# Optimization experiments

Hardware: AMD Instinct MI355X
Metric: run time of the kernel (lower is better)

## Reference

```python
import jax, jax.numpy as jnp
import numpy as np

NUM_CLASSES = 80
SCORE_THR = 0.2
NMS_THR = 0.3
MAX_PER_IMAGE = 100
TOPK_PER_CLASS = 100  # cap on pre-NMS candidates per (image, class); >= max_per_image
ANCHOR_MASK = [[6, 7, 8], [3, 4, 5], [0, 1, 2]]
COCO_ANCHORS = np.array([[10, 13], [16, 30], [33, 23], [30, 61], [62, 45],
                         [59, 119], [116, 90], [156, 198], [373, 326]], dtype=np.float32)


def yolo_head(feats, layer_anchors, num_classes, input_shape):
    # feats: [B, 3*(5+C), gh, gw]
    B = feats.shape[0]
    gh, gw = feats.shape[2], feats.shape[3]
    na = layer_anchors.shape[0]
    f = feats.reshape(B, na, num_classes + 5, gh, gw).transpose(0, 3, 4, 1, 2)  # [B,gh,gw,3,5+C]
    gy, gx = jnp.meshgrid(jnp.arange(gh), jnp.arange(gw), indexing='ij')
    grid = jnp.stack([gx, gy], axis=-1).astype(f.dtype)[None, :, :, None, :]  # [1,gh,gw,1,2]
    # literal translation: divide by tensor([gh, gw]) (square grids in practice)
    box_xy = (jax.nn.sigmoid(f[..., :2]) + grid) / jnp.array([gh, gw], f.dtype)
    box_wh = jnp.exp(f[..., 2:4]) * layer_anchors[None, None, None, :, :] / input_shape[None, None, None, None, :]
    conf = jax.nn.sigmoid(f[..., 4:5])
    probs = jax.nn.sigmoid(f[..., 5:])
    return box_xy, box_wh, conf, probs


def yolo_correct_boxes(box_xy, box_wh, input_shape, image_shape):
    box_yx = box_xy[..., ::-1]
    box_hw = box_wh[..., ::-1]
    new_shape = jnp.round(image_shape * jnp.min(input_shape / image_shape))
    offset = (input_shape - new_shape) / 2.0 / input_shape
    scale = input_shape / new_shape
    box_yx = (box_yx - offset) * scale
    box_hw = box_hw * scale
    mins = box_yx - box_hw / 2.0
    maxes = box_yx + box_hw / 2.0
    boxes = jnp.concatenate([mins, maxes], axis=-1)  # (ymin, xmin, ymax, xmax)
    return boxes * jnp.concatenate([image_shape, image_shape])


def decode_layer(feats, layer_anchors, input_shape, image_shape):
    box_xy, box_wh, conf, probs = yolo_head(feats, layer_anchors, NUM_CLASSES, input_shape)
    boxes = yolo_correct_boxes(box_xy, box_wh, input_shape, image_shape)  # [B,gh,gw,3,4]
    B = feats.shape[0]
    return boxes.reshape(B, -1, 4), (conf * probs).reshape(B, -1, NUM_CLASSES)


def pairwise_iou(b):
    # b: [K,4] (y1,x1,y2,x2)
    y1, x1, y2, x2 = b[:, 0], b[:, 1], b[:, 2], b[:, 3]
    area = jnp.maximum(y2 - y1, 0) * jnp.maximum(x2 - x1, 0)
    iy1 = jnp.maximum(y1[:, None], y1[None, :])
    ix1 = jnp.maximum(x1[:, None], x1[None, :])
    iy2 = jnp.minimum(y2[:, None], y2[None, :])
    ix2 = jnp.minimum(x2[:, None], x2[None, :])
    inter = jnp.maximum(iy2 - iy1, 0) * jnp.maximum(ix2 - ix1, 0)
    return inter / (area[:, None] + area[None, :] - inter + 1e-9)


def greedy_nms(boxes, valid):
    # boxes [K,4] sorted by descending score; valid [K] bool. Returns keep mask [K].
    K = boxes.shape[0]
    iou = jax.lax.stop_gradient(pairwise_iou(boxes))
    idx = jnp.arange(K)
    def body(i, sup):
        keep_i = valid[i] & (~sup[i])
        return sup | (keep_i & (iou[i] > NMS_THR) & (idx > i))
    sup = jax.lax.fori_loop(0, K, body, jnp.zeros((K,), bool))
    return valid & (~sup)


def setup_inputs() -> dict:
    key = jax.random.key(0)
    k0, k1, k2 = jax.random.split(key, 3)
    B, F = 16, 3 * (5 + NUM_CLASSES)
    feat0 = jax.random.normal(k0, (B, F, 19, 19), jnp.float32)
    feat1 = jax.random.normal(k1, (B, F, 38, 38), jnp.float32)
    feat2 = jax.random.normal(k2, (B, F, 76, 76), jnp.float32)
    anchors = jnp.asarray(COCO_ANCHORS)
    image_shape = jnp.array([480.0, 640.0], jnp.float32)
    return {"feat0": feat0, "feat1": feat1, "feat2": feat2,
            "anchors": anchors, "image_shape": image_shape}


def reference(feat0, feat1, feat2, anchors, image_shape):
    input_shape = jnp.array([feat0.shape[2] * 32, feat0.shape[3] * 32], jnp.float32)
    feats = [feat0, feat1, feat2]
    boxes_l, scores_l = [], []
    for l in range(3):
        b, s = decode_layer(feats[l], anchors[np.array(ANCHOR_MASK[l])], input_shape, image_shape)
        boxes_l.append(b)
        scores_l.append(s)
    boxes = jnp.concatenate(boxes_l, axis=1)    # [B,N,4]
    scores = jnp.concatenate(scores_l, axis=1)  # [B,N,C]
    B = scores.shape[0]
    sc = scores.transpose(0, 2, 1)              # [B,C,N]
    top_s, top_i = jax.lax.top_k(sc, TOPK_PER_CLASS)              # [B,C,K]
    top_b = jnp.take_along_axis(boxes[:, None, :, :], top_i[..., None], axis=2)  # [B,C,K,4]
    valid = top_s >= SCORE_THR
    keep = jax.vmap(jax.vmap(greedy_nms))(top_b, valid)           # [B,C,K]
    cand = jnp.where(keep, top_s, -1.0)
    flat_s = cand.reshape(B, -1)                 # [B, C*K]
    flat_b = top_b.reshape(B, -1, 4)
    sel_s, sel_i = jax.lax.top_k(flat_s, MAX_PER_IMAGE)           # [B,100]
    sel_b = jnp.take_along_axis(flat_b, sel_i[..., None], axis=1)  # [B,100,4]
    sel_c = (sel_i // TOPK_PER_CLASS).astype(jnp.float32)
    # dets: (ymin, xmin, ymax, xmax, score, class); score == -1 marks padding
    return jnp.concatenate([sel_b, sel_s[..., None], sel_c[..., None]], axis=-1)
```

## Files before the change

kernel.cpp:

```cpp
#include <hip/hip_runtime.h>
#include <hip/hip_bf16.h>


#define NTOT   22743
#define NCLS   80
#define TOPK   100
#define KPAD   22752
#define NG2    2166
#define Q_L1   17328
#define Q_L0   21660
#define SCORE_THR 0.2f
#define NMS_THR   0.3f

__device__ __forceinline__ float sig_exact(float x) {
    return 1.0f / (1.0f + expf(-x));
}
__device__ __forceinline__ float sig_fast(float x) {
    return __builtin_amdgcn_rcpf(1.0f + __expf(-x));
}

__global__ __launch_bounds__(256) void k_decode(
    const float* __restrict__ f0, const float* __restrict__ f1,
    const float* __restrict__ f2, const float* __restrict__ anchors,
    const float* __restrict__ imshape, float4* __restrict__ boxes,
    float* __restrict__ conf_q, int total) {
    int gid = blockIdx.x * 256 + threadIdx.x;
    if (gid >= total) return;
    int b = gid / NTOT; int p = gid - b * NTOT;

    const float* f; int ghw, gw, l, off, a, s;
    if (p < 1083)      { f=f0; off=0;    ghw=361;  gw=19; l=0; int r=p;      a=r/361;  s=r-a*361;  }
    else if (p < 5415) { f=f1; off=1083; ghw=1444; gw=38; l=1; int r=p-1083; a=r/1444; s=r-a*1444; }
    else               { f=f2; off=5415; ghw=5776; gw=76; l=2; int r=p-5415; a=r/5776; s=r-a*5776; }
    int y = s / gw, x = s - y * gw;

    const float* q = f + ((size_t)(b * 255 + a * 85) * ghw + s);
    float tx = q[0], ty = q[ghw], tw = q[2*ghw], th = q[3*ghw], tc = q[4*ghw];

    int arow = (2 - l) * 3 + a;
    float aw = anchors[arow * 2], ah = anchors[arow * 2 + 1];
    float imh = imshape[0], imw = imshape[1];
    float gf = (float)gw;

    float bxx = (sig_exact(tx) + (float)x) / gf;
    float bxy = (sig_exact(ty) + (float)y) / gf;
    float bw  = expf(tw) * aw / 608.0f;
    float bh  = expf(th) * ah / 608.0f;

    float r  = fminf(608.0f / imh, 608.0f / imw);
    float nh = rintf(imh * r), nw = rintf(imw * r);
    float offy = (608.0f - nh) / 2.0f / 608.0f;
    float offx = (608.0f - nw) / 2.0f / 608.0f;
    float scy = 608.0f / nh, scx = 608.0f / nw;

    float cy = (bxy - offy) * scy;
    float cx = (bxx - offx) * scx;
    float hh = bh * scy, ww = bw * scx;

    int n = off + 3 * s + a;
    boxes[(size_t)b * NTOT + n] =
        make_float4((cy - hh / 2.0f) * imh, (cx - ww / 2.0f) * imw,
                    (cy + hh / 2.0f) * imh, (cx + ww / 2.0f) * imw);
    int qi = (l == 2) ? (a * 5776 + s)
           : (l == 1) ? (Q_L1 + a * 1444 + s)
                      : (Q_L0 + a * 361 + s);
    conf_q[(size_t)b * KPAD + qi] = sig_exact(tc);
}

__device__ void find_pivot(unsigned* hist, int H, unsigned target,
                           unsigned* suf, unsigned* sh_p, unsigned* sh_above) {
    const int tid = threadIdx.x;
    const int per = H >> 8;
    if (tid < 256) {
        unsigned acc = 0;
        for (int u = 0; u < per; ++u) acc += hist[tid * per + u];
        suf[tid] = acc;
    }
    __syncthreads();
    for (int off = 1; off < 256; off <<= 1) {
        unsigned v = 0;
        if (tid < 256) v = (tid + off < 256) ? suf[tid + off] : 0u;
        __syncthreads();
        if (tid < 256) suf[tid] += v;
        __syncthreads();
    }
    if (tid < 256) {
        unsigned mysuf = suf[tid];
        unsigned nxt = (tid == 255) ? 0u : suf[tid + 1];
        if (mysuf >= target && nxt < target) {
            unsigned above = nxt;
            for (int h = tid * per + per - 1; h >= tid * per; --h) {
                unsigned c2 = above + hist[h];
                if (c2 >= target) { *sh_p = (unsigned)h; *sh_above = above; break; }
                above = c2;
            }
        }
    }
    __syncthreads();
}

__device__ __forceinline__ unsigned pack2(float cfa, float lga, float cfb, float lgb) {
    unsigned ka = __float_as_uint(cfa * sig_fast(lga)) >> 16;
    unsigned kb = __float_as_uint(cfb * sig_fast(lgb)) >> 16;
    return ka | (kb << 16);
}

__device__ __forceinline__ void collect_cand(
    int b, int c, int q, const float* __restrict__ f0,
    const float* __restrict__ f1, const float* __restrict__ f2,
    const float* __restrict__ conf_q, unsigned long long* buf,
    unsigned* sh_cnt) {
    int a, s, nbase, ghw;
    const float* f;
    if (q < Q_L1)      { a = q / 5776;  s = q - a * 5776;  f = f2; ghw = 5776; nbase = 5415; }
    else if (q < Q_L0) { int r = q - Q_L1; a = r / 1444; s = r - a * 1444; f = f1; ghw = 1444; nbase = 1083; }
    else               { int r = q - Q_L0; a = r / 361;  s = r - a * 361;  f = f0; ghw = 361;  nbase = 0;    }
    float t  = f[((size_t)(b * 255 + a * 85 + 5 + c)) * ghw + s];
    float cf = conf_q[(size_t)b * KPAD + q];
    float sce = cf * sig_exact(t);
    int n = nbase + 3 * s + a;
    unsigned slot = atomicAdd(sh_cnt, 1u);
    if (slot < 512)
        buf[slot] = (((unsigned long long)__float_as_uint(sce)) << 32)
                    | (unsigned)(~n);
}

__global__ __launch_bounds__(512, 4) void k_topk(
    const float* __restrict__ f0, const float* __restrict__ f1,
    const float* __restrict__ f2, const float* __restrict__ conf_q,
    const float4* __restrict__ boxes, float4* __restrict__ top_b,
    float* __restrict__ cand) {
    __shared__ unsigned int histp[4096];
    __shared__ unsigned long long buf[512];
    __shared__ unsigned int wsum[4];
    __shared__ float sb_y1[TOPK], sb_x1[TOPK], sb_y2[TOPK], sb_x2[TOPK], sb_s[TOPK];
    __shared__ unsigned int sh_p, sh_cnt;

    const int tid = threadIdx.x;
    const int row = blockIdx.x;
    const int b = row / NCLS, c = row - b * NCLS;
    const float* cq = conf_q + (size_t)b * KPAD;

    for (int i = tid; i < 4096; i += 512) histp[i] = 0;
    if (tid == 0) sh_cnt = 0;

    uint4 v[5];
    bool  val[5];
    float4 lg0[5], lg1[5], cf0[5], cf1[5];
    #pragma unroll
    for (int k = 0; k < 5; ++k) {
        int g = tid + k * 512;
        val[k] = (g < NG2);
        if (val[k]) {
            int q = g * 8;
            int a = q / 5776, s = q - a * 5776;
            const float* fp = f2 + ((size_t)(b * 255 + a * 85 + 5 + c)) * 5776 + s;
            lg0[k] = *(const float4*)fp;
            lg1[k] = *(const float4*)(fp + 4);
            cf0[k] = *(const float4*)(cq + q);
            cf1[k] = *(const float4*)(cq + q + 4);
        }
    }
    #pragma unroll
    for (int k = 0; k < 5; ++k) {
        if (val[k]) {
            v[k].x = pack2(cf0[k].x, lg0[k].x, cf0[k].y, lg0[k].y);
            v[k].y = pack2(cf0[k].z, lg0[k].z, cf0[k].w, lg0[k].w);
            v[k].z = pack2(cf1[k].x, lg1[k].x, cf1[k].y, lg1[k].y);
            v[k].w = pack2(cf1[k].z, lg1[k].z, cf1[k].w, lg1[k].w);
        } else v[k] = make_uint4(0, 0, 0, 0);
    }

    const bool lv = (tid < 361);
    unsigned k1p[6];
    if (lv) {
        float4 l1g[3], l1c[3];
        #pragma unroll
        for (int p = 0; p < 3; ++p) {
            const float* fp = f1 + ((size_t)(b * 255 + p * 85 + 5 + c)) * 1444 + 4 * tid;
            l1g[p] = *(const float4*)fp;
            l1c[p] = *(const float4*)(cq + Q_L1 + p * 1444 + 4 * tid);
        }
        #pragma unroll
        for (int p = 0; p < 3; ++p) {
            k1p[2*p]   = pack2(l1c[p].x, l1g[p].x, l1c[p].y, l1g[p].y);
            k1p[2*p+1] = pack2(l1c[p].z, l1g[p].z, l1c[p].w, l1g[p].w);
        }
    }

    unsigned k0[3];
    if (lv) {
        float g0f[3], c0f[3];
        #pragma unroll
        for (int p = 0; p < 3; ++p) {
            g0f[p] = f0[((size_t)(b * 255 + p * 85 + 5 + c)) * 361 + tid];
            c0f[p] = cq[Q_L0 + p * 361 + tid];
        }
        #pragma unroll
        for (int p = 0; p < 3; ++p)
            k0[p] = __float_as_uint(c0f[p] * sig_fast(g0f[p])) >> 16;
    }
    __syncthreads();

    #pragma unroll
    for (int k = 0; k < 5; ++k) if (val[k]) {
        unsigned ks[8] = { v[k].x & 0xFFFFu, v[k].x >> 16, v[k].y & 0xFFFFu, v[k].y >> 16,
                           v[k].z & 0xFFFFu, v[k].z >> 16, v[k].w & 0xFFFFu, v[k].w >> 16 };
        #pragma unroll
        for (int j = 0; j < 8; ++j)
            atomicAdd(&histp[ks[j] >> 2], 1u << (((ks[j] >> 1) & 1u) * 16));
    }
    if (lv) {
        #pragma unroll
        for (int p = 0; p < 3; ++p) {
            unsigned ks[4] = { k1p[2*p] & 0xFFFFu, k1p[2*p] >> 16,
                               k1p[2*p+1] & 0xFFFFu, k1p[2*p+1] >> 16 };
            #pragma unroll
            for (int j = 0; j < 4; ++j)
                atomicAdd(&histp[ks[j] >> 2], 1u << (((ks[j] >> 1) & 1u) * 16));
            atomicAdd(&histp[k0[p] >> 2], 1u << (((k0[p] >> 1) & 1u) * 16));
        }
    }
    __syncthreads();

    {
        const int lane = tid & 63;
        unsigned own = 0;
        if (tid < 256) {
            #pragma unroll
            for (int u = 0; u < 16; ++u) {
                unsigned w = histp[tid * 16 + u];
                own += (w & 0xFFFFu) + (w >> 16);
            }
        }
        unsigned acc = own;
        #pragma unroll
        for (int d = 1; d < 64; d <<= 1) {
            unsigned vv = __shfl_down(acc, d, 64);
            if (lane + d < 64) acc += vv;
        }
        if (tid < 256 && lane == 0) wsum[tid >> 6] = acc;
        __syncthreads();
        if (tid < 256) {
            unsigned tail = 0;
            for (int w2 = (tid >> 6) + 1; w2 < 4; ++w2) tail += wsum[w2];
            unsigned suft = acc + tail;
            unsigned nxt  = suft - own;
            if (suft >= TOPK && nxt < TOPK) {
                unsigned above = nxt;
                for (int bb = 31; bb >= 0; --bb) {
                    unsigned w = histp[tid * 16 + (bb >> 1)];
                    unsigned cnt = (bb & 1) ? (w >> 16) : (w & 0xFFFFu);
                    if (above + cnt >= TOPK) { sh_p = (unsigned)(tid * 32 + bb); break; }
                    above += cnt;
                }
            }
        }
        __syncthreads();
    }
    const unsigned kthr = sh_p > 0 ? ((sh_p - 1) << 1) : 0u;

    #pragma unroll
    for (int k = 0; k < 5; ++k) if (val[k]) {
        unsigned ks[8] = { v[k].x & 0xFFFFu, v[k].x >> 16, v[k].y & 0xFFFFu, v[k].y >> 16,
                           v[k].z & 0xFFFFu, v[k].z >> 16, v[k].w & 0xFFFFu, v[k].w >> 16 };
        #pragma unroll
        for (int j = 0; j < 8; ++j)
            if (ks[j] >= kthr)
                collect_cand(b, c, (tid + k * 512) * 8 + j, f0, f1, f2, conf_q, buf, &sh_cnt);
    }
    if (lv) {
        #pragma unroll
        for (int p = 0; p < 3; ++p) {
            unsigned ks[4] = { k1p[2*p] & 0xFFFFu, k1p[2*p] >> 16,
                               k1p[2*p+1] & 0xFFFFu, k1p[2*p+1] >> 16 };
            #pragma unroll
            for (int j = 0; j < 4; ++j)
                if (ks[j] >= kthr)
                    collect_cand(b, c, Q_L1 + p * 1444 + 4 * tid + j, f0, f1, f2, conf_q, buf, &sh_cnt);
            if (k0[p] >= kthr)
                collect_cand(b, c, Q_L0 + p * 361 + tid, f0, f1, f2, conf_q, buf, &sh_cnt);
        }
    }
    __syncthreads();

    const int M = (int)min(sh_cnt, 512u);
    if (tid < M) {
        unsigned long long mykey = buf[tid];
        int rank = 0;
        for (int j = 0; j < M; ++j) rank += (buf[j] > mykey);
        if (rank < TOPK) {
            int n = (int)(~(unsigned)mykey);
            float4 bx = boxes[(size_t)b * NTOT + n];
            sb_y1[rank] = bx.x; sb_x1[rank] = bx.y;
            sb_y2[rank] = bx.z; sb_x2[rank] = bx.w;
            sb_s[rank]  = __uint_as_float((unsigned)(mykey >> 32));
            top_b[(size_t)row * TOPK + rank] = bx;
        }
    }
    __syncthreads();

    if (tid < 64) {
        const int j0 = tid, j1 = tid + 64;
        const bool v1 = (j1 < TOPK);
        float y10 = sb_y1[j0], x10 = sb_x1[j0], y20 = sb_y2[j0], x20 = sb_x2[j0];
        float s0 = sb_s[j0];
        float y11 = v1 ? sb_y1[j1] : 0.f, x11 = v1 ? sb_x1[j1] : 0.f;
        float y21 = v1 ? sb_y2[j1] : 0.f, x21 = v1 ? sb_x2[j1] : 0.f;
        float s1 = v1 ? sb_s[j1] : -1.0f;
        float ar0 = fmaxf(y20 - y10, 0.f) * fmaxf(x20 - x10, 0.f);
        float ar1 = fmaxf(y21 - y11, 0.f) * fmaxf(x21 - x11, 0.f);
        int sup0 = 0, sup1 = 0;
        for (int i = 0; i < TOPK; ++i) {
            float yi1 = sb_y1[i], xi1 = sb_x1[i], yi2 = sb_y2[i], xi2 = sb_x2[i];
            float si = sb_s[i];
            int supi = (i < 64) ? __shfl(sup0, i, 64) : __shfl(sup1, i - 64, 64);
            bool keep_i = (si >= SCORE_THR) && (supi == 0);
            if (keep_i) {
                float ari = fmaxf(yi2 - yi1, 0.f) * fmaxf(xi2 - xi1, 0.f);
                if (j0 > i) {
                    float ty1 = fmaxf(yi1, y10), tx1 = fmaxf(xi1, x10);
                    float ty2 = fminf(yi2, y20), tx2 = fminf(xi2, x20);
                    float inter = fmaxf(ty2 - ty1, 0.f) * fmaxf(tx2 - tx1, 0.f);
                    float iou = inter / (ari + ar0 - inter + 1e-9f);
                    if (iou > NMS_THR) sup0 = 1;
                }
                if (v1 && j1 > i) {
                    float ty1 = fmaxf(yi1, y11), tx1 = fmaxf(xi1, x11);
                    float ty2 = fminf(yi2, y21), tx2 = fminf(xi2, x21);
                    float inter = fmaxf(ty2 - ty1, 0.f) * fmaxf(tx2 - tx1, 0.f);
                    float iou = inter / (ari + ar1 - inter + 1e-9f);
                    if (iou > NMS_THR) sup1 = 1;
                }
            }
        }
        cand[(size_t)row * TOPK + j0] = (s0 >= SCORE_THR && sup0 == 0) ? s0 : -1.0f;
        if (v1)
            cand[(size_t)row * TOPK + j1] = (s1 >= SCORE_THR && sup1 == 0) ? s1 : -1.0f;
    }
}

__global__ __launch_bounds__(256) void k_final(
    const float* __restrict__ cand, const float4* __restrict__ top_b,
    float* __restrict__ out) {
    __shared__ float cs[8000];
    __shared__ unsigned int hist[4096];
    __shared__ unsigned long long buf[512];
    __shared__ unsigned int suf[256];
    __shared__ unsigned int sh_kp, sh_p1, sh_above1, sh_p2, sh_above2, sh_cnt;

    const int tid = threadIdx.x, b = blockIdx.x;
    if (tid == 0) { sh_kp = 0; sh_cnt = 0; }
    for (int i = tid; i < 4096; i += 256) hist[i] = 0;
    __syncthreads();

    unsigned lk = 0;
    for (int i = tid; i < 8000; i += 256) {
        float v = cand[b * 8000 + i];
        cs[i] = v;
        if (v > -0.5f) lk++;
    }
    atomicAdd(&sh_kp, lk);
    __syncthreads();
    unsigned Kp = sh_kp;

    if (Kp >= TOPK) {
        for (int i = tid; i < 8000; i += 256)
            if (cs[i] > -0.5f) atomicAdd(&hist[__float_as_uint(cs[i]) >> 19], 1u);
        __syncthreads();
        find_pivot(hist, 2048, TOPK, suf, &sh_p1, &sh_above1);
        unsigned p1 = sh_p1, above1 = sh_above1;
        for (int i = tid; i < 4096; i += 256) hist[i] = 0;
        __syncthreads();
        for (int i = tid; i < 8000; i += 256) {
            float v = cs[i];
            if (v > -0.5f) {
                unsigned bits = __float_as_uint(v);
                if ((bits >> 19) == p1) atomicAdd(&hist[(bits >> 7) & 0xFFFu], 1u);
            }
        }
        __syncthreads();
        find_pivot(hist, 4096, TOPK - above1, suf, &sh_p2, &sh_above2);
        unsigned p2 = sh_p2;
        for (int i = tid; i < 8000; i += 256) {
            float v = cs[i];
            if (v > -0.5f) {
                unsigned bits = __float_as_uint(v);
                unsigned b1 = bits >> 19;
                if (b1 > p1 || (b1 == p1 && ((bits >> 7) & 0xFFFu) >= p2)) {
                    unsigned slot = atomicAdd(&sh_cnt, 1u);
                    if (slot < 512)
                        buf[slot] = (((unsigned long long)bits) << 32) | (unsigned)(~i);
                }
            }
        }
    } else {
        for (int i = tid; i < 8000; i += 256) {
            float v = cs[i];
            if (v > -0.5f) {
                unsigned slot = atomicAdd(&sh_cnt, 1u);
                buf[slot] = (((unsigned long long)__float_as_uint(v)) << 32) | (unsigned)(~i);
            }
        }
        __syncthreads();
        if (tid == 0) {
            unsigned need = TOPK - Kp, got = 0;
            for (int i = 0; i < 8000 && got < need; ++i)
                if (cs[i] <= -0.5f) { buf[Kp + got] = (unsigned)(~i); got++; }
        }
    }
    __syncthreads();

    const int M2 = (Kp >= TOPK) ? (int)min(sh_cnt, 512u) : (int)TOPK;
    for (int i = tid; i < M2; i += 256) {
        unsigned long long key = buf[i];
        int rank = 0;
        for (int j = 0; j < M2; ++j) rank += (buf[j] > key);
        if (rank < TOPK) {
            int fi = (int)(~(unsigned)key);
            int c = fi / TOPK; int kk = fi - c * TOPK;
            float4 bb = top_b[((size_t)b * NCLS + c) * TOPK + kk];
            int base = (b * TOPK + rank) * 6;
            out[base + 0] = bb.x; out[base + 1] = bb.y;
            out[base + 2] = bb.z; out[base + 3] = bb.w;
            out[base + 4] = cs[fi]; out[base + 5] = (float)c;
        }
    }
}

extern "C" void kernel_launch(void* const* d_in, const int* in_sizes, int n_in,
                              void* d_out, int out_size, void* d_ws, size_t ws_size,
                              hipStream_t stream) {
    (void)n_in; (void)out_size; (void)ws_size;
    const float* f0      = (const float*)d_in[0];
    const float* f1      = (const float*)d_in[1];
    const float* f2      = (const float*)d_in[2];
    const float* anchors = (const float*)d_in[3];
    const float* imshape = (const float*)d_in[4];
    const int B = in_sizes[0] / (255 * 19 * 19);

    char* ws = (char*)d_ws;
    size_t o = 0;
    float4* boxes  = (float4*)(ws + o); o += (size_t)B * NTOT * sizeof(float4);
    float*  conf_q = (float*)(ws + o);  o += (size_t)B * KPAD * sizeof(float);
    float4* top_b  = (float4*)(ws + o); o += (size_t)B * NCLS * TOPK * sizeof(float4);
    float*  cand   = (float*)(ws + o);  o += (size_t)B * NCLS * TOPK * sizeof(float);
    float*  out    = (float*)d_out;

    const int total = B * NTOT;
    k_decode<<<(total + 255) / 256, 256, 0, stream>>>(f0, f1, f2, anchors, imshape,
                                                      boxes, conf_q, total);
    k_topk<<<B * NCLS, 512, 0, stream>>>(f0, f1, f2, conf_q, boxes,
                                         top_b, cand);
    k_final<<<B, 256, 0, stream>>>(cand, top_b, out);
}
```

Baseline: 262.0 us.

## Fuse decode, per-class top-k/NMS and final selection into one kernel

Removes the separate decode kernel: objectness sigmoid is recomputed from raw features inside each class block, and box decoding runs only for the selected top-100 candidates. The final per-image selection kernel is folded in through an atomic last-block-done counter with threadfences, leaving one memset and one launch. This drops the boxes and conf_q workspace traffic and two launches. In exchange every class block rereads the objectness plane and redoes its sigmoid, and one block per image serialises the final merge at the tail.

Result: slower. 376.3 us (+43.6%).

```diff
diff --git a/kernel.cpp b/kernel.cpp
--- a/kernel.cpp
+++ b/kernel.cpp
@@ -1,11 +1,9 @@
 #include <hip/hip_runtime.h>
-#include <hip/hip_bf16.h>
 
 
 #define NTOT   22743
 #define NCLS   80
 #define TOPK   100
-#define KPAD   22752
 #define NG2    2166
 #define Q_L1   17328
 #define Q_L0   21660
@@ -18,53 +16,10 @@
 __device__ __forceinline__ float sig_fast(float x) {
     return __builtin_amdgcn_rcpf(1.0f + __expf(-x));
 }
-
-__global__ __launch_bounds__(256) void k_decode(
-    const float* __restrict__ f0, const float* __restrict__ f1,
-    const float* __restrict__ f2, const float* __restrict__ anchors,
-    const float* __restrict__ imshape, float4* __restrict__ boxes,
-    float* __restrict__ conf_q, int total) {
-    int gid = blockIdx.x * 256 + threadIdx.x;
-    if (gid >= total) return;
-    int b = gid / NTOT; int p = gid - b * NTOT;
-
-    const float* f; int ghw, gw, l, off, a, s;
-    if (p < 1083)      { f=f0; off=0;    ghw=361;  gw=19; l=0; int r=p;      a=r/361;  s=r-a*361;  }
-    else if (p < 5415) { f=f1; off=1083; ghw=1444; gw=38; l=1; int r=p-1083; a=r/1444; s=r-a*1444; }
-    else               { f=f2; off=5415; ghw=5776; gw=76; l=2; int r=p-5415; a=r/5776; s=r-a*5776; }
-    int y = s / gw, x = s - y * gw;
-
-    const float* q = f + ((size_t)(b * 255 + a * 85) * ghw + s);
-    float tx = q[0], ty = q[ghw], tw = q[2*ghw], th = q[3*ghw], tc = q[4*ghw];
-
-    int arow = (2 - l) * 3 + a;
-    float aw = anchors[arow * 2], ah = anchors[arow * 2 + 1];
-    float imh = imshape[0], imw = imshape[1];
-    float gf = (float)gw;
-
-    float bxx = (sig_exact(tx) + (float)x) / gf;
-    float bxy = (sig_exact(ty) + (float)y) / gf;
-    float bw  = expf(tw) * aw / 608.0f;
-    float bh  = expf(th) * ah / 608.0f;
-
-    float r  = fminf(608.0f / imh, 608.0f / imw);
-    float nh = rintf(imh * r), nw = rintf(imw * r);
-    float offy = (608.0f - nh) / 2.0f / 608.0f;
-    float offx = (608.0f - nw) / 2.0f / 608.0f;
-    float scy = 608.0f / nh, scx = 608.0f / nw;
-
-    float cy = (bxy - offy) * scy;
-    float cx = (bxx - offx) * scx;
-    float hh = bh * scy, ww = bw * scx;
-
-    int n = off + 3 * s + a;
-    boxes[(size_t)b * NTOT + n] =
-        make_float4((cy - hh / 2.0f) * imh, (cx - ww / 2.0f) * imw,
-                    (cy + hh / 2.0f) * imh, (cx + ww / 2.0f) * imw);
-    int qi = (l == 2) ? (a * 5776 + s)
-           : (l == 1) ? (Q_L1 + a * 1444 + s)
-                      : (Q_L0 + a * 361 + s);
-    conf_q[(size_t)b * KPAD + qi] = sig_exact(tc);
+__device__ __forceinline__ unsigned pack2(float cfa, float lga, float cfb, float lgb) {
+    unsigned ka = __float_as_uint(cfa * sig_fast(lga)) >> 16;
+    unsigned kb = __float_as_uint(cfb * sig_fast(lgb)) >> 16;
+    return ka | (kb << 16);
 }
 
 __device__ void find_pivot(unsigned* hist, int H, unsigned target,
@@ -99,25 +54,19 @@
     __syncthreads();
 }
 
-__device__ __forceinline__ unsigned pack2(float cfa, float lga, float cfb, float lgb) {
-    unsigned ka = __float_as_uint(cfa * sig_fast(lga)) >> 16;
-    unsigned kb = __float_as_uint(cfb * sig_fast(lgb)) >> 16;
-    return ka | (kb << 16);
-}
-
 __device__ __forceinline__ void collect_cand(
     int b, int c, int q, const float* __restrict__ f0,
     const float* __restrict__ f1, const float* __restrict__ f2,
-    const float* __restrict__ conf_q, unsigned long long* buf,
-    unsigned* sh_cnt) {
+    unsigned long long* buf, unsigned* sh_cnt) {
     int a, s, nbase, ghw;
     const float* f;
     if (q < Q_L1)      { a = q / 5776;  s = q - a * 5776;  f = f2; ghw = 5776; nbase = 5415; }
     else if (q < Q_L0) { int r = q - Q_L1; a = r / 1444; s = r - a * 1444; f = f1; ghw = 1444; nbase = 1083; }
     else               { int r = q - Q_L0; a = r / 361;  s = r - a * 361;  f = f0; ghw = 361;  nbase = 0;    }
-    float t  = f[((size_t)(b * 255 + a * 85 + 5 + c)) * ghw + s];
-    float cf = conf_q[(size_t)b * KPAD + q];
-    float sce = cf * sig_exact(t);
+    const float* pl = f + ((size_t)(b * 255 + a * 85)) * ghw + s;
+    float t  = pl[(size_t)(5 + c) * ghw];
+    float tc = pl[(size_t)4 * ghw];
+    float sce = sig_exact(tc) * sig_exact(t);
     int n = nbase + 3 * s + a;
     unsigned slot = atomicAdd(sh_cnt, 1u);
     if (slot < 512)
@@ -125,80 +74,92 @@
                     | (unsigned)(~n);
 }
 
-__global__ __launch_bounds__(512, 4) void k_topk(
+__global__ __launch_bounds__(512, 4) void k_one(
     const float* __restrict__ f0, const float* __restrict__ f1,
-    const float* __restrict__ f2, const float* __restrict__ conf_q,
-    const float4* __restrict__ boxes, float4* __restrict__ top_b,
-    float* __restrict__ cand) {
+    const float* __restrict__ f2, const float* __restrict__ anchors,
+    const float* __restrict__ imshape, float4* __restrict__ top_b,
+    float* __restrict__ cand, unsigned* __restrict__ ctr,
+    float* __restrict__ out) {
     __shared__ unsigned int histp[4096];
     __shared__ unsigned long long buf[512];
     __shared__ unsigned int wsum[4];
     __shared__ float sb_y1[TOPK], sb_x1[TOPK], sb_y2[TOPK], sb_x2[TOPK], sb_s[TOPK];
-    __shared__ unsigned int sh_p, sh_cnt;
+    __shared__ unsigned int suf2[256];
+    __shared__ unsigned int sh_p, sh_cnt, sh_last, sh_kp, sh_p1, sh_ab1, sh_p2, sh_ab2;
 
     const int tid = threadIdx.x;
     const int row = blockIdx.x;
     const int b = row / NCLS, c = row - b * NCLS;
-    const float* cq = conf_q + (size_t)b * KPAD;
 
     for (int i = tid; i < 4096; i += 512) histp[i] = 0;
     if (tid == 0) sh_cnt = 0;
 
     uint4 v[5];
     bool  val[5];
-    float4 lg0[5], lg1[5], cf0[5], cf1[5];
-    #pragma unroll
-    for (int k = 0; k < 5; ++k) {
-        int g = tid + k * 512;
-        val[k] = (g < NG2);
-        if (val[k]) {
-            int q = g * 8;
-            int a = q / 5776, s = q - a * 5776;
-            const float* fp = f2 + ((size_t)(b * 255 + a * 85 + 5 + c)) * 5776 + s;
-            lg0[k] = *(const float4*)fp;
-            lg1[k] = *(const float4*)(fp + 4);
-            cf0[k] = *(const float4*)(cq + q);
-            cf1[k] = *(const float4*)(cq + q + 4);
-        }
-    }
-    #pragma unroll
-    for (int k = 0; k < 5; ++k) {
-        if (val[k]) {
-            v[k].x = pack2(cf0[k].x, lg0[k].x, cf0[k].y, lg0[k].y);
-            v[k].y = pack2(cf0[k].z, lg0[k].z, cf0[k].w, lg0[k].w);
-            v[k].z = pack2(cf1[k].x, lg1[k].x, cf1[k].y, lg1[k].y);
-            v[k].w = pack2(cf1[k].z, lg1[k].z, cf1[k].w, lg1[k].w);
-        } else v[k] = make_uint4(0, 0, 0, 0);
+    {
+        float4 lg0[5], lg1[5], ct0[5], ct1[5];
+        #pragma unroll
+        for (int k = 0; k < 5; ++k) {
+            int g = tid + k * 512;
+            val[k] = (g < NG2);
+            if (val[k]) {
+                int q = g * 8;
+                int a = q / 5776, s = q - a * 5776;
+                const float* base2 = f2 + ((size_t)(b * 255 + a * 85)) * 5776 + s;
+                lg0[k] = *(const float4*)(base2 + (size_t)(5 + c) * 5776);
+                lg1[k] = *(const float4*)(base2 + (size_t)(5 + c) * 5776 + 4);
+                ct0[k] = *(const float4*)(base2 + (size_t)4 * 5776);
+                ct1[k] = *(const float4*)(base2 + (size_t)4 * 5776 + 4);
+            }
+        }
+        #pragma unroll
+        for (int k = 0; k < 5; ++k) {
+            if (val[k]) {
+                float4 c0, c1;
+                c0.x = sig_exact(ct0[k].x); c0.y = sig_exact(ct0[k].y);
+                c0.z = sig_exact(ct0[k].z); c0.w = sig_exact(ct0[k].w);
+                c1.x = sig_exact(ct1[k].x); c1.y = sig_exact(ct1[k].y);
+                c1.z = sig_exact(ct1[k].z); c1.w = sig_exact(ct1[k].w);
+                v[k].x = pack2(c0.x, lg0[k].x, c0.y, lg0[k].y);
+                v[k].y = pack2(c0.z, lg0[k].z, c0.w, lg0[k].w);
+                v[k].z = pack2(c1.x, lg1[k].x, c1.y, lg1[k].y);
+                v[k].w = pack2(c1.z, lg1[k].z, c1.w, lg1[k].w);
+            } else v[k] = make_uint4(0, 0, 0, 0);
+        }
     }
 
     const bool lv = (tid < 361);
     unsigned k1p[6];
     if (lv) {
-        float4 l1g[3], l1c[3];
+        float4 l1g[3], l1t[3];
         #pragma unroll
         for (int p = 0; p < 3; ++p) {
-            const float* fp = f1 + ((size_t)(b * 255 + p * 85 + 5 + c)) * 1444 + 4 * tid;
-            l1g[p] = *(const float4*)fp;
-            l1c[p] = *(const float4*)(cq + Q_L1 + p * 1444 + 4 * tid);
+            const float* base1 = f1 + ((size_t)(b * 255 + p * 85)) * 1444 + 4 * tid;
+            l1g[p] = *(const float4*)(base1 + (size_t)(5 + c) * 1444);
+            l1t[p] = *(const float4*)(base1 + (size_t)4 * 1444);
         }
         #pragma unroll
         for (int p = 0; p < 3; ++p) {
-            k1p[2*p]   = pack2(l1c[p].x, l1g[p].x, l1c[p].y, l1g[p].y);
-            k1p[2*p+1] = pack2(l1c[p].z, l1g[p].z, l1c[p].w, l1g[p].w);
+            float4 cf;
+            cf.x = sig_exact(l1t[p].x); cf.y = sig_exact(l1t[p].y);
+            cf.z = sig_exact(l1t[p].z); cf.w = sig_exact(l1t[p].w);
+            k1p[2*p]   = pack2(cf.x, l1g[p].x, cf.y, l1g[p].y);
+            k1p[2*p+1] = pack2(cf.z, l1g[p].z, cf.w, l1g[p].w);
         }
     }
 
     unsigned k0[3];
     if (lv) {
-        float g0f[3], c0f[3];
+        float g0f[3], t0f[3];
         #pragma unroll
         for (int p = 0; p < 3; ++p) {
-            g0f[p] = f0[((size_t)(b * 255 + p * 85 + 5 + c)) * 361 + tid];
-            c0f[p] = cq[Q_L0 + p * 361 + tid];
+            const float* base0 = f0 + ((size_t)(b * 255 + p * 85)) * 361 + tid;
+            g0f[p] = base0[(size_t)(5 + c) * 361];
+            t0f[p] = base0[(size_t)4 * 361];
         }
         #pragma unroll
         for (int p = 0; p < 3; ++p)
-            k0[p] = __float_as_uint(c0f[p] * sig_fast(g0f[p])) >> 16;
+            k0[p] = __float_as_uint(sig_exact(t0f[p]) * sig_fast(g0f[p])) >> 16;
     }
     __syncthreads();
 
@@ -267,7 +228,7 @@
         #pragma unroll
         for (int j = 0; j < 8; ++j)
             if (ks[j] >= kthr)
-                collect_cand(b, c, (tid + k * 512) * 8 + j, f0, f1, f2, conf_q, buf, &sh_cnt);
+                collect_cand(b, c, (tid + k * 512) * 8 + j, f0, f1, f2, buf, &sh_cnt);
     }
     if (lv) {
         #pragma unroll
@@ -277,9 +238,9 @@
             #pragma unroll
             for (int j = 0; j < 4; ++j)
                 if (ks[j] >= kthr)
-                    collect_cand(b, c, Q_L1 + p * 1444 + 4 * tid + j, f0, f1, f2, conf_q, buf, &sh_cnt);
+                    collect_cand(b, c, Q_L1 + p * 1444 + 4 * tid + j, f0, f1, f2, buf, &sh_cnt);
             if (k0[p] >= kthr)
-                collect_cand(b, c, Q_L0 + p * 361 + tid, f0, f1, f2, conf_q, buf, &sh_cnt);
+                collect_cand(b, c, Q_L0 + p * 361 + tid, f0, f1, f2, buf, &sh_cnt);
         }
     }
     __syncthreads();
@@ -290,8 +251,34 @@
         int rank = 0;
         for (int j = 0; j < M; ++j) rank += (buf[j] > mykey);
         if (rank < TOPK) {
-            int n = (int)(~(unsigned)mykey);
-            float4 bx = boxes[(size_t)b * NTOT + n];
+            int nn = (int)(~(unsigned)mykey);
+            const float* f; int ghw, gw, l, off;
+            if (nn < 1083)      { f = f0; off = 0;    ghw = 361;  gw = 19; l = 0; }
+            else if (nn < 5415) { f = f1; off = 1083; ghw = 1444; gw = 38; l = 1; }
+            else                { f = f2; off = 5415; ghw = 5776; gw = 76; l = 2; }
+            int m2 = nn - off; int a = m2 % 3; int s = m2 / 3;
+            int y = s / gw, x = s - y * gw;
+            const float* qp = f + ((size_t)(b * 255 + a * 85)) * ghw + s;
+            float tx = qp[0], ty = qp[(size_t)ghw];
+            float tw = qp[2 * (size_t)ghw], th = qp[3 * (size_t)ghw];
+            int arow = (2 - l) * 3 + a;
+            float aw = anchors[arow * 2], ah = anchors[arow * 2 + 1];
+            float imh = imshape[0], imw = imshape[1];
+            float gf = (float)gw;
+            float bxx = (sig_exact(tx) + (float)x) / gf;
+            float bxy = (sig_exact(ty) + (float)y) / gf;
+            float bw  = expf(tw) * aw / 608.0f;
+            float bh  = expf(th) * ah / 608.0f;
+            float r  = fminf(608.0f / imh, 608.0f / imw);
+            float nh = rintf(imh * r), nw2 = rintf(imw * r);
+            float offy = (608.0f - nh) / 2.0f / 608.0f;
+            float offx = (608.0f - nw2) / 2.0f / 608.0f;
+            float scy = 608.0f / nh, scx = 608.0f / nw2;
+            float cy = (bxy - offy) * scy;
+            float cx = (bxx - offx) * scx;
+            float hh = bh * scy, ww = bw * scx;
+            float4 bx = make_float4((cy - hh / 2.0f) * imh, (cx - ww / 2.0f) * imw,
+                                    (cy + hh / 2.0f) * imh, (cx + ww / 2.0f) * imw);
             sb_y1[rank] = bx.x; sb_x1[rank] = bx.y;
             sb_y2[rank] = bx.z; sb_x2[rank] = bx.w;
             sb_s[rank]  = __uint_as_float((unsigned)(mykey >> 32));
@@ -338,92 +325,91 @@
         if (v1)
             cand[(size_t)row * TOPK + j1] = (s1 >= SCORE_THR && sup1 == 0) ? s1 : -1.0f;
     }
-}
-
-__global__ __launch_bounds__(256) void k_final(
-    const float* __restrict__ cand, const float4* __restrict__ top_b,
-    float* __restrict__ out) {
-    __shared__ float cs[8000];
-    __shared__ unsigned int hist[4096];
-    __shared__ unsigned long long buf[512];
-    __shared__ unsigned int suf[256];
-    __shared__ unsigned int sh_kp, sh_p1, sh_above1, sh_p2, sh_above2, sh_cnt;
-
-    const int tid = threadIdx.x, b = blockIdx.x;
-    if (tid == 0) { sh_kp = 0; sh_cnt = 0; }
-    for (int i = tid; i < 4096; i += 256) hist[i] = 0;
-    __syncthreads();
-
-    unsigned lk = 0;
-    for (int i = tid; i < 8000; i += 256) {
-        float v = cand[b * 8000 + i];
-        cs[i] = v;
-        if (v > -0.5f) lk++;
-    }
-    atomicAdd(&sh_kp, lk);
-    __syncthreads();
-    unsigned Kp = sh_kp;
-
-    if (Kp >= TOPK) {
-        for (int i = tid; i < 8000; i += 256)
-            if (cs[i] > -0.5f) atomicAdd(&hist[__float_as_uint(cs[i]) >> 19], 1u);
-        __syncthreads();
-        find_pivot(hist, 2048, TOPK, suf, &sh_p1, &sh_above1);
-        unsigned p1 = sh_p1, above1 = sh_above1;
-        for (int i = tid; i < 4096; i += 256) hist[i] = 0;
-        __syncthreads();
-        for (int i = tid; i < 8000; i += 256) {
-            float v = cs[i];
-            if (v > -0.5f) {
-                unsigned bits = __float_as_uint(v);
-                if ((bits >> 19) == p1) atomicAdd(&hist[(bits >> 7) & 0xFFFu], 1u);
-            }
-        }
-        __syncthreads();
-        find_pivot(hist, 4096, TOPK - above1, suf, &sh_p2, &sh_above2);
-        unsigned p2 = sh_p2;
-        for (int i = tid; i < 8000; i += 256) {
-            float v = cs[i];
-            if (v > -0.5f) {
-                unsigned bits = __float_as_uint(v);
-                unsigned b1 = bits >> 19;
-                if (b1 > p1 || (b1 == p1 && ((bits >> 7) & 0xFFFu) >= p2)) {
+    __syncthreads();
+
+    if (tid == 0) {
+        __threadfence();
+        unsigned old = atomicAdd(&ctr[b], 1u);
+        sh_last = (old == NCLS - 1) ? 1u : 0u;
+    }
+    __syncthreads();
+    if (sh_last) {
+        __threadfence();
+        const float* cb = cand + (size_t)b * (NCLS * TOPK);
+        for (int i = tid; i < 4096; i += 512) histp[i] = 0;
+        if (tid == 0) { sh_kp = 0; sh_cnt = 0; }
+        __syncthreads();
+
+        unsigned lk = 0;
+        for (int i = tid; i < 8000; i += 512)
+            if (cb[i] > -0.5f) lk++;
+        atomicAdd(&sh_kp, lk);
+        __syncthreads();
+        unsigned Kp = sh_kp;
+
+        if (Kp >= TOPK) {
+            for (int i = tid; i < 8000; i += 512) {
+                float vv = cb[i];
+                if (vv > -0.5f) atomicAdd(&histp[__float_as_uint(vv) >> 19], 1u);
+            }
+            __syncthreads();
+            find_pivot(histp, 2048, TOPK, suf2, &sh_p1, &sh_ab1);
+            unsigned p1 = sh_p1, above1 = sh_ab1;
+            for (int i = tid; i < 4096; i += 512) histp[i] = 0;
+            __syncthreads();
+            for (int i = tid; i < 8000; i += 512) {
+                float vv = cb[i];
+                if (vv > -0.5f) {
+                    unsigned bits = __float_as_uint(vv);
+                    if ((bits >> 19) == p1) atomicAdd(&histp[(bits >> 7) & 0xFFFu], 1u);
+                }
+            }
+            __syncthreads();
+            find_pivot(histp, 4096, TOPK - above1, suf2, &sh_p2, &sh_ab2);
+            unsigned p2 = sh_p2;
+            for (int i = tid; i < 8000; i += 512) {
+                float vv = cb[i];
+                if (vv > -0.5f) {
+                    unsigned bits = __float_as_uint(vv);
+                    unsigned b1 = bits >> 19;
+                    if (b1 > p1 || (b1 == p1 && ((bits >> 7) & 0xFFFu) >= p2)) {
+                        unsigned slot = atomicAdd(&sh_cnt, 1u);
+                        if (slot < 512)
+                            buf[slot] = (((unsigned long long)bits) << 32) | (unsigned)(~i);
+                    }
+                }
+            }
+        } else {
+            for (int i = tid; i < 8000; i += 512) {
+                float vv = cb[i];
+                if (vv > -0.5f) {
                     unsigned slot = atomicAdd(&sh_cnt, 1u);
-                    if (slot < 512)
-                        buf[slot] = (((unsigned long long)bits) << 32) | (unsigned)(~i);
-                }
-            }
-        }
-    } else {
-        for (int i = tid; i < 8000; i += 256) {
-            float v = cs[i];
-            if (v > -0.5f) {
-                unsigned slot = atomicAdd(&sh_cnt, 1u);
-                buf[slot] = (((unsigned long long)__float_as_uint(v)) << 32) | (unsigned)(~i);
-            }
-        }
-        __syncthreads();
-        if (tid == 0) {
-            unsigned need = TOPK - Kp, got = 0;
-            for (int i = 0; i < 8000 && got < need; ++i)
-                if (cs[i] <= -0.5f) { buf[Kp + got] = (unsigned)(~i); got++; }
-        }
-    }
-    __syncthreads();
-
-    const int M2 = (Kp >= TOPK) ? (int)min(sh_cnt, 512u) : (int)TOPK;
-    for (int i = tid; i < M2; i += 256) {
-        unsigned long long key = buf[i];
-        int rank = 0;
-        for (int j = 0; j < M2; ++j) rank += (buf[j] > key);
-        if (rank < TOPK) {
-            int fi = (int)(~(unsigned)key);
-            int c = fi / TOPK; int kk = fi - c * TOPK;
-            float4 bb = top_b[((size_t)b * NCLS + c) * TOPK + kk];
-            int base = (b * TOPK + rank) * 6;
-            out[base + 0] = bb.x; out[base + 1] = bb.y;
-            out[base + 2] = bb.z; out[base + 3] = bb.w;
-            out[base + 4] = cs[fi]; out[base + 5] = (float)c;
+                    buf[slot] = (((unsigned long long)__float_as_uint(vv)) << 32) | (unsigned)(~i);
+                }
+            }
+            __syncthreads();
+            if (tid == 0) {
+                unsigned need = TOPK - Kp, got = 0;
+                for (int i = 0; i < 8000 && got < need; ++i)
+                    if (cb[i] <= -0.5f) { buf[Kp + got] = (unsigned)(~i); got++; }
+            }
+        }
+        __syncthreads();
+
+        const int M2 = (Kp >= TOPK) ? (int)min(sh_cnt, 512u) : (int)TOPK;
+        for (int i = tid; i < M2; i += 512) {
+            unsigned long long key = buf[i];
+            int rank = 0;
+            for (int j = 0; j < M2; ++j) rank += (buf[j] > key);
+            if (rank < TOPK) {
+                int fi = (int)(~(unsigned)key);
+                int cc = fi / TOPK; int kk = fi - cc * TOPK;
+                float4 bb = top_b[((size_t)b * NCLS + cc) * TOPK + kk];
+                int base = (b * TOPK + rank) * 6;
+                out[base + 0] = bb.x; out[base + 1] = bb.y;
+                out[base + 2] = bb.z; out[base + 3] = bb.w;
+                out[base + 4] = cb[fi]; out[base + 5] = (float)cc;
+            }
         }
     }
 }
@@ -441,16 +427,12 @@
 
     char* ws = (char*)d_ws;
     size_t o = 0;
-    float4* boxes  = (float4*)(ws + o); o += (size_t)B * NTOT * sizeof(float4);
-    float*  conf_q = (float*)(ws + o);  o += (size_t)B * KPAD * sizeof(float);
-    float4* top_b  = (float4*)(ws + o); o += (size_t)B * NCLS * TOPK * sizeof(float4);
-    float*  cand   = (float*)(ws + o);  o += (size_t)B * NCLS * TOPK * sizeof(float);
-    float*  out    = (float*)d_out;
-
-    const int total = B * NTOT;
-    k_decode<<<(total + 255) / 256, 256, 0, stream>>>(f0, f1, f2, anchors, imshape,
-                                                      boxes, conf_q, total);
-    k_topk<<<B * NCLS, 512, 0, stream>>>(f0, f1, f2, conf_q, boxes,
-                                         top_b, cand);
-    k_final<<<B, 256, 0, stream>>>(cand, top_b, out);
-}
+    float4*   top_b = (float4*)(ws + o);   o += (size_t)B * NCLS * TOPK * sizeof(float4);
+    float*    cand  = (float*)(ws + o);    o += (size_t)B * NCLS * TOPK * sizeof(float);
+    unsigned* ctr   = (unsigned*)(ws + o); o += (size_t)B * sizeof(unsigned);
+    float*    out   = (float*)d_out;
+
+    hipMemsetAsync(ctr, 0, (size_t)B * sizeof(unsigned), stream);
+    k_one<<<B * NCLS, 512, 0, stream>>>(f0, f1, f2, anchors, imshape,
+                                        top_b, cand, ctr, out);
+}
```
